# Kernel optimization log

Measured on AMD Instinct MI355X. Metric: run time of the kernel, lower is better.

The kernel has to match this reference:

```python
import jax, jax.numpy as jnp
import numpy as np

STATE_DIM = 1024
INPUT_DIM = 1024
OUTPUT_DIM = 1024
BATCH = 8
SEQ = 2048


def setup_inputs() -> dict:
    key = jax.random.key(0)
    k_x, k_a, k_b, k_w, k_bias = jax.random.split(key, 5)
    x = jax.random.normal(k_x, (BATCH, SEQ, INPUT_DIM), dtype=jnp.float32)
    # diagonal transition a in (0, 0.99) for stability
    A = jax.random.uniform(k_a, (STATE_DIM,), dtype=jnp.float32, minval=0.0, maxval=0.99)
    B = jax.random.normal(k_b, (STATE_DIM, INPUT_DIM), dtype=jnp.float32) / np.sqrt(INPUT_DIM)
    W = jax.random.normal(k_w, (OUTPUT_DIM, STATE_DIM), dtype=jnp.float32) / np.sqrt(STATE_DIM)
    b = jax.random.normal(k_bias, (OUTPUT_DIM,), dtype=jnp.float32) * 0.01
    return {"x": x, "A": A, "B": B, "W": W, "b": b}


def reference(x, A, B, W, b):
    # x: [batch, seq, input_dim]
    # Input projection: u_t = B x_t  -> [batch, seq, state_dim]
    u = jnp.einsum('bld,nd->bln', x, B)
    # Diagonal linear recurrence h_t = A * h_{t-1} + u_t via associative scan.
    # Pair representation (a, b) composes as (a1*a2, a2*b1 + b2).
    aa = jnp.broadcast_to(A, u.shape)

    def combine(c1, c2):
        a1, b1 = c1
        a2, b2 = c2
        return a1 * a2, a2 * b1 + b2

    _, h = jax.lax.associative_scan(combine, (aa, u), axis=1)
    # Output projection: [batch, seq, output_dim]
    return jnp.einsum('bln,on->blo', h, W) + b
```

## Files before the change

### kernel.cpp

```cpp
#include <hip/hip_runtime.h>
#include <stdint.h>

#define BATCH 8
#define SEQ 2048
#define DIM 1024
#define MTOT (BATCH * SEQ)
#define NCHUNK 32
#define CLEN (SEQ / NCHUNK)

typedef __attribute__((ext_vector_type(8))) short short8;
typedef __attribute__((ext_vector_type(4))) float floatx4;


__device__ __forceinline__ unsigned short f2bf(float f) {
  union { float f; unsigned u; } c; c.f = f;
  unsigned u = c.u;
  return (unsigned short)((u + 0x7FFFu + ((u >> 16) & 1u)) >> 16);
}
__device__ __forceinline__ float bf2f(unsigned short h) {
  union { unsigned u; float f; } c; c.u = ((unsigned)h) << 16;
  return c.f;
}

__device__ __forceinline__ void gll16(const void* g, void* l) {
  __builtin_amdgcn_global_load_lds(
      (__attribute__((address_space(1))) void*)(uintptr_t)g,
      (__attribute__((address_space(3))) void*)(uintptr_t)l,
      16, 0, 0);
}


__global__ __launch_bounds__(256) void cast_f32_bf16_kernel(
    const float* __restrict__ src, unsigned short* __restrict__ dst, int n8) {
  int i = blockIdx.x * 256 + threadIdx.x;
  if (i >= n8) return;
  const float4* s4 = (const float4*)src;
  float4 a = s4[2 * i], b = s4[2 * i + 1];
  uint4 o;
  o.x = (unsigned)f2bf(a.x) | ((unsigned)f2bf(a.y) << 16);
  o.y = (unsigned)f2bf(a.z) | ((unsigned)f2bf(a.w) << 16);
  o.z = (unsigned)f2bf(b.x) | ((unsigned)f2bf(b.y) << 16);
  o.w = (unsigned)f2bf(b.z) | ((unsigned)f2bf(b.w) << 16);
  ((uint4*)dst)[i] = o;
}


template <bool OUT_BF16>
__global__ __launch_bounds__(256) void gemm_nt(
    const unsigned short* __restrict__ A,
    const unsigned short* __restrict__ B,
    void* __restrict__ Cp,
    const float* __restrict__ bias,
    int K, int N) {
  __shared__ unsigned short sA[128 * 64];
  __shared__ unsigned short sB[128 * 64];

  const int tid = threadIdx.x;
  const int wave = tid >> 6, lane = tid & 63;
  const size_t m0 = (size_t)blockIdx.y * 128;
  const int n0 = blockIdx.x * 128;

  floatx4 acc[4][4] = {};

  const int srow = wave * 8 + (lane >> 3);
  const int scol = (lane & 7) * 8;
  const unsigned short* gA = A + (m0 + srow) * (size_t)K + scol;
  const unsigned short* gB = B + ((size_t)n0 + srow) * (size_t)K + scol;
  unsigned short* lA = sA + wave * 8 * 64;
  unsigned short* lB = sB + wave * 8 * 64;

  const int fr = lane & 15;
  const int fk = (lane >> 4) * 8;
  const int wm = (wave & 1) * 64, wn = (wave >> 1) * 64;

  for (int kt = 0; kt < K; kt += 64) {
#pragma unroll
    for (int r = 0; r < 4; ++r) {
      gll16(gA + (size_t)r * 32 * K + kt, lA + r * 32 * 64);
      gll16(gB + (size_t)r * 32 * K + kt, lB + r * 32 * 64);
    }
    asm volatile("s_waitcnt vmcnt(0)" ::: "memory");
    __syncthreads();
#pragma unroll
    for (int kk = 0; kk < 64; kk += 32) {
      short8 af[4], bfv[4];
#pragma unroll
      for (int i = 0; i < 4; ++i)
        af[i] = *(const short8*)(sA + (wm + i * 16 + fr) * 64 + kk + fk);
#pragma unroll
      for (int j = 0; j < 4; ++j)
        bfv[j] = *(const short8*)(sB + (wn + j * 16 + fr) * 64 + kk + fk);
#pragma unroll
      for (int i = 0; i < 4; ++i)
#pragma unroll
        for (int j = 0; j < 4; ++j)
          acc[i][j] = __builtin_amdgcn_mfma_f32_16x16x32_bf16(
              af[i], bfv[j], acc[i][j], 0, 0, 0);
    }
    __syncthreads();
  }

  const int col = lane & 15;
  const int row4 = (lane >> 4) * 4;
#pragma unroll
  for (int i = 0; i < 4; ++i) {
#pragma unroll
    for (int j = 0; j < 4; ++j) {
#pragma unroll
      for (int r = 0; r < 4; ++r) {
        size_t m = m0 + wm + i * 16 + row4 + r;
        int n = n0 + wn + j * 16 + col;
        float v = acc[i][j][r];
        if (OUT_BF16) {
          ((unsigned short*)Cp)[m * N + n] = f2bf(v);
        } else {
          ((float*)Cp)[m * N + n] = v + bias[n];
        }
      }
    }
  }
}


__global__ __launch_bounds__(256) void scan_carry(
    const unsigned short* __restrict__ u, const float* __restrict__ A,
    float* __restrict__ carry) {
  const int n = blockIdx.x * 256 + threadIdx.x;
  const int c = blockIdx.y;
  const int b = blockIdx.z;
  const float a = A[n];
  size_t base = ((size_t)(b * SEQ + c * CLEN)) * DIM + n;
  float s = 0.f;
#pragma unroll 8
  for (int t = 0; t < CLEN; ++t)
    s = fmaf(a, s, bf2f(u[base + (size_t)t * DIM]));
  carry[((size_t)b * NCHUNK + c) * DIM + n] = s;
}

__global__ __launch_bounds__(256) void scan_combine(
    float* __restrict__ carry, const float* __restrict__ A) {
  const int id = blockIdx.x * 256 + threadIdx.x;
  const int b = id >> 10, n = id & (DIM - 1);
  float a = A[n];
  float aL = a;
#pragma unroll
  for (int i = 0; i < 6; ++i) aL *= aL;
  float s = 0.f;
  for (int c = 0; c < NCHUNK; ++c) {
    size_t idx = ((size_t)b * NCHUNK + c) * DIM + n;
    float local = carry[idx];
    carry[idx] = s;
    s = fmaf(aL, s, local);
  }
}

__global__ __launch_bounds__(256) void scan_apply(
    unsigned short* __restrict__ u, const float* __restrict__ A,
    const float* __restrict__ carry) {
  const int n = blockIdx.x * 256 + threadIdx.x;
  const int c = blockIdx.y;
  const int b = blockIdx.z;
  const float a = A[n];
  float s = carry[((size_t)b * NCHUNK + c) * DIM + n];
  size_t base = ((size_t)(b * SEQ + c * CLEN)) * DIM + n;
#pragma unroll 8
  for (int t = 0; t < CLEN; ++t) {
    size_t idx = base + (size_t)t * DIM;
    s = fmaf(a, s, bf2f(u[idx]));
    u[idx] = f2bf(s);
  }
}


extern "C" void kernel_launch(void* const* d_in, const int* in_sizes, int n_in,
                              void* d_out, int out_size, void* d_ws,
                              size_t ws_size, hipStream_t stream) {
  const float* x    = (const float*)d_in[0];
  const float* A    = (const float*)d_in[1];
  const float* B    = (const float*)d_in[2];
  const float* W    = (const float*)d_in[3];
  const float* bias = (const float*)d_in[4];

  char* ws = (char*)d_ws;
  unsigned short* xb = (unsigned short*)ws;
  unsigned short* u  = (unsigned short*)(ws + 33554432);
  unsigned short* Bb = (unsigned short*)(ws + 67108864);
  unsigned short* Wb = (unsigned short*)(ws + 69206016);
  float* carry       = (float*)(ws + 71303168);

  cast_f32_bf16_kernel<<<(MTOT * DIM / 8) / 256, 256, 0, stream>>>(
      x, xb, MTOT * DIM / 8);
  cast_f32_bf16_kernel<<<(DIM * DIM / 8) / 256, 256, 0, stream>>>(
      B, Bb, DIM * DIM / 8);
  cast_f32_bf16_kernel<<<(DIM * DIM / 8) / 256, 256, 0, stream>>>(
      W, Wb, DIM * DIM / 8);

  gemm_nt<true><<<dim3(DIM / 128, MTOT / 128), 256, 0, stream>>>(
      xb, Bb, (void*)u, nullptr, DIM, DIM);

  scan_carry<<<dim3(DIM / 256, NCHUNK, BATCH), 256, 0, stream>>>(u, A, carry);
  scan_combine<<<dim3((BATCH * DIM) / 256), 256, 0, stream>>>(carry, A);
  scan_apply<<<dim3(DIM / 256, NCHUNK, BATCH), 256, 0, stream>>>(u, A, carry);

  gemm_nt<false><<<dim3(DIM / 128, MTOT / 128), 256, 0, stream>>>(
      u, Wb, d_out, bias, DIM, DIM);
}
```

Before: 257.7 us.

## Fuse casts, swizzle GEMM LDS, remap tiles per XCD, vectorize scan kernels

Merges the three cast kernels into one launch. The GEMM gets an XOR-swizzled LDS layout to cut bank conflicts, a 1D grid remapped so each XCD owns contiguous M tiles for L2 reuse, and a bf16 epilogue staged through LDS for coalesced 16-byte stores. The scan kernels now process 8 channels per thread with vector loads and stores, and the chunk count doubles to expose more parallelism. The carry buffer reuses the xb workspace region, which is safe only because xb is dead after the first GEMM.

```diff
diff --git a/kernel.cpp b/kernel.cpp
--- a/kernel.cpp
+++ b/kernel.cpp
@@ -5,10 +5,11 @@
 #define SEQ 2048
 #define DIM 1024
 #define MTOT (BATCH * SEQ)
-#define NCHUNK 32
+#define NCHUNK 64
 #define CLEN (SEQ / NCHUNK)
 
 typedef __attribute__((ext_vector_type(8))) short short8;
+typedef __attribute__((ext_vector_type(8))) unsigned short ushort8;
 typedef __attribute__((ext_vector_type(4))) float floatx4;
 
 
@@ -30,18 +31,32 @@
 }
 
 
-__global__ __launch_bounds__(256) void cast_f32_bf16_kernel(
-    const float* __restrict__ src, unsigned short* __restrict__ dst, int n8) {
+#define XN8 (MTOT * DIM / 8)
+#define MN8 (DIM * DIM / 8)
+
+__global__ __launch_bounds__(256) void cast3_kernel(
+    const float* __restrict__ x, const float* __restrict__ B,
+    const float* __restrict__ W, unsigned short* __restrict__ xb,
+    unsigned short* __restrict__ Bb, unsigned short* __restrict__ Wb) {
   int i = blockIdx.x * 256 + threadIdx.x;
-  if (i >= n8) return;
+  const float* src;
+  unsigned short* dst;
+  int li;
+  if (i < XN8) {
+    src = x; dst = xb; li = i;
+  } else if (i < XN8 + MN8) {
+    src = B; dst = Bb; li = i - XN8;
+  } else {
+    src = W; dst = Wb; li = i - XN8 - MN8;
+  }
   const float4* s4 = (const float4*)src;
-  float4 a = s4[2 * i], b = s4[2 * i + 1];
+  float4 a = s4[2 * li], b = s4[2 * li + 1];
   uint4 o;
   o.x = (unsigned)f2bf(a.x) | ((unsigned)f2bf(a.y) << 16);
   o.y = (unsigned)f2bf(a.z) | ((unsigned)f2bf(a.w) << 16);
   o.z = (unsigned)f2bf(b.x) | ((unsigned)f2bf(b.y) << 16);
   o.w = (unsigned)f2bf(b.z) | ((unsigned)f2bf(b.w) << 16);
-  ((uint4*)dst)[i] = o;
+  ((uint4*)dst)[li] = o;
 }
 
 
@@ -52,25 +67,32 @@
     void* __restrict__ Cp,
     const float* __restrict__ bias,
     int K, int N) {
-  __shared__ unsigned short sA[128 * 64];
-  __shared__ unsigned short sB[128 * 64];
+  __shared__ unsigned short smem[16384];
+  unsigned short* sA = smem;
+  unsigned short* sB = smem + 8192;
 
   const int tid = threadIdx.x;
   const int wave = tid >> 6, lane = tid & 63;
-  const size_t m0 = (size_t)blockIdx.y * 128;
-  const int n0 = blockIdx.x * 128;
+
+  const int id = blockIdx.x;
+  const int xcd = id & 7, j = id >> 3;
+  const int mt = xcd * 16 + (j >> 3);
+  const int nt = j & 7;
+  const size_t m0 = (size_t)mt * 128;
+  const int n0 = nt * 128;
 
   floatx4 acc[4][4] = {};
 
   const int srow = wave * 8 + (lane >> 3);
-  const int scol = (lane & 7) * 8;
+  const int scol = (((lane & 7) ^ ((lane >> 3) & 7)) * 8);
   const unsigned short* gA = A + (m0 + srow) * (size_t)K + scol;
   const unsigned short* gB = B + ((size_t)n0 + srow) * (size_t)K + scol;
   unsigned short* lA = sA + wave * 8 * 64;
   unsigned short* lB = sB + wave * 8 * 64;
 
   const int fr = lane & 15;
-  const int fk = (lane >> 4) * 8;
+  const int frs = fr & 7;
+  const int kb = lane >> 4;
   const int wm = (wave & 1) * 64, wn = (wave >> 1) * 64;
 
   for (int kt = 0; kt < K; kt += 64) {
@@ -86,35 +108,55 @@
       short8 af[4], bfv[4];
 #pragma unroll
       for (int i = 0; i < 4; ++i)
-        af[i] = *(const short8*)(sA + (wm + i * 16 + fr) * 64 + kk + fk);
-#pragma unroll
-      for (int j = 0; j < 4; ++j)
-        bfv[j] = *(const short8*)(sB + (wn + j * 16 + fr) * 64 + kk + fk);
+        af[i] = *(const short8*)(sA + (wm + i * 16 + fr) * 64 +
+                                 ((((kk >> 3) + kb) ^ frs) * 8));
+#pragma unroll
+      for (int jj = 0; jj < 4; ++jj)
+        bfv[jj] = *(const short8*)(sB + (wn + jj * 16 + fr) * 64 +
+                                   ((((kk >> 3) + kb) ^ frs) * 8));
 #pragma unroll
       for (int i = 0; i < 4; ++i)
 #pragma unroll
-        for (int j = 0; j < 4; ++j)
-          acc[i][j] = __builtin_amdgcn_mfma_f32_16x16x32_bf16(
-              af[i], bfv[j], acc[i][j], 0, 0, 0);
+        for (int jj = 0; jj < 4; ++jj)
+          acc[i][jj] = __builtin_amdgcn_mfma_f32_16x16x32_bf16(
+              af[i], bfv[jj], acc[i][jj], 0, 0, 0);
     }
     __syncthreads();
   }
 
   const int col = lane & 15;
   const int row4 = (lane >> 4) * 4;
-#pragma unroll
-  for (int i = 0; i < 4; ++i) {
-#pragma unroll
-    for (int j = 0; j < 4; ++j) {
-#pragma unroll
-      for (int r = 0; r < 4; ++r) {
-        size_t m = m0 + wm + i * 16 + row4 + r;
-        int n = n0 + wn + j * 16 + col;
-        float v = acc[i][j][r];
-        if (OUT_BF16) {
-          ((unsigned short*)Cp)[m * N + n] = f2bf(v);
-        } else {
-          ((float*)Cp)[m * N + n] = v + bias[n];
+
+  if (OUT_BF16) {
+    unsigned short* sC = smem;
+#pragma unroll
+    for (int i = 0; i < 4; ++i)
+#pragma unroll
+      for (int jj = 0; jj < 4; ++jj)
+#pragma unroll
+        for (int r = 0; r < 4; ++r)
+          sC[(wm + i * 16 + row4 + r) * 128 + wn + jj * 16 + col] =
+              f2bf(acc[i][jj][r]);
+    __syncthreads();
+    unsigned short* C = (unsigned short*)Cp;
+#pragma unroll
+    for (int s = 0; s < 8; ++s) {
+      int row = wave * 32 + s * 4 + (lane >> 4);
+      int c8 = (lane & 15) * 8;
+      *(ushort8*)(C + (m0 + row) * (size_t)N + n0 + c8) =
+          *(const ushort8*)(sC + row * 128 + c8);
+    }
+  } else {
+    float* C = (float*)Cp;
+#pragma unroll
+    for (int i = 0; i < 4; ++i) {
+#pragma unroll
+      for (int jj = 0; jj < 4; ++jj) {
+#pragma unroll
+        for (int r = 0; r < 4; ++r) {
+          size_t m = m0 + wm + i * 16 + row4 + r;
+          int n = n0 + wn + jj * 16 + col;
+          C[m * N + n] = acc[i][jj][r] + bias[n];
         }
       }
     }
@@ -125,16 +167,24 @@
 __global__ __launch_bounds__(256) void scan_carry(
     const unsigned short* __restrict__ u, const float* __restrict__ A,
     float* __restrict__ carry) {
-  const int n = blockIdx.x * 256 + threadIdx.x;
-  const int c = blockIdx.y;
-  const int b = blockIdx.z;
-  const float a = A[n];
-  size_t base = ((size_t)(b * SEQ + c * CLEN)) * DIM + n;
-  float s = 0.f;
-#pragma unroll 8
-  for (int t = 0; t < CLEN; ++t)
-    s = fmaf(a, s, bf2f(u[base + (size_t)t * DIM]));
-  carry[((size_t)b * NCHUNK + c) * DIM + n] = s;
+  const int n0 = threadIdx.x * 8;
+  const int c = blockIdx.x * 2 + threadIdx.y;
+  const int b = blockIdx.y;
+  float a[8], s[8];
+  *(float4*)&a[0] = *(const float4*)(A + n0);
+  *(float4*)&a[4] = *(const float4*)(A + n0 + 4);
+#pragma unroll
+  for (int i = 0; i < 8; ++i) s[i] = 0.f;
+  size_t base = ((size_t)(b * SEQ + c * CLEN)) * DIM + n0;
+#pragma unroll 4
+  for (int t = 0; t < CLEN; ++t) {
+    ushort8 v = *(const ushort8*)(u + base + (size_t)t * DIM);
+#pragma unroll
+    for (int i = 0; i < 8; ++i) s[i] = fmaf(a[i], s[i], bf2f(v[i]));
+  }
+  float* dst = carry + ((size_t)b * NCHUNK + c) * DIM + n0;
+  *(float4*)dst = *(float4*)&s[0];
+  *(float4*)(dst + 4) = *(float4*)&s[4];
 }
 
 __global__ __launch_bounds__(256) void scan_combine(
@@ -144,7 +194,7 @@
   float a = A[n];
   float aL = a;
 #pragma unroll
-  for (int i = 0; i < 6; ++i) aL *= aL;
+  for (int i = 0; i < 5; ++i) aL *= aL;
   float s = 0.f;
   for (int c = 0; c < NCHUNK; ++c) {
     size_t idx = ((size_t)b * NCHUNK + c) * DIM + n;
@@ -157,17 +207,27 @@
 __global__ __launch_bounds__(256) void scan_apply(
     unsigned short* __restrict__ u, const float* __restrict__ A,
     const float* __restrict__ carry) {
-  const int n = blockIdx.x * 256 + threadIdx.x;
-  const int c = blockIdx.y;
-  const int b = blockIdx.z;
-  const float a = A[n];
-  float s = carry[((size_t)b * NCHUNK + c) * DIM + n];
-  size_t base = ((size_t)(b * SEQ + c * CLEN)) * DIM + n;
-#pragma unroll 8
+  const int n0 = threadIdx.x * 8;
+  const int c = blockIdx.x * 2 + threadIdx.y;
+  const int b = blockIdx.y;
+  float a[8], s[8];
+  *(float4*)&a[0] = *(const float4*)(A + n0);
+  *(float4*)&a[4] = *(const float4*)(A + n0 + 4);
+  const float* cin = carry + ((size_t)b * NCHUNK + c) * DIM + n0;
+  *(float4*)&s[0] = *(const float4*)cin;
+  *(float4*)&s[4] = *(const float4*)(cin + 4);
+  size_t base = ((size_t)(b * SEQ + c * CLEN)) * DIM + n0;
+#pragma unroll 4
   for (int t = 0; t < CLEN; ++t) {
     size_t idx = base + (size_t)t * DIM;
-    s = fmaf(a, s, bf2f(u[idx]));
-    u[idx] = f2bf(s);
+    ushort8 v = *(const ushort8*)(u + idx);
+    ushort8 o;
+#pragma unroll
+    for (int i = 0; i < 8; ++i) {
+      s[i] = fmaf(a[i], s[i], bf2f(v[i]));
+      o[i] = f2bf(s[i]);
+    }
+    *(ushort8*)(u + idx) = o;
   }
 }
 
@@ -183,25 +243,20 @@
 
   char* ws = (char*)d_ws;
   unsigned short* xb = (unsigned short*)ws;
+  float* carry       = (float*)ws;
   unsigned short* u  = (unsigned short*)(ws + 33554432);
   unsigned short* Bb = (unsigned short*)(ws + 67108864);
   unsigned short* Wb = (unsigned short*)(ws + 69206016);
-  float* carry       = (float*)(ws + 71303168);
-
-  cast_f32_bf16_kernel<<<(MTOT * DIM / 8) / 256, 256, 0, stream>>>(
-      x, xb, MTOT * DIM / 8);
-  cast_f32_bf16_kernel<<<(DIM * DIM / 8) / 256, 256, 0, stream>>>(
-      B, Bb, DIM * DIM / 8);
-  cast_f32_bf16_kernel<<<(DIM * DIM / 8) / 256, 256, 0, stream>>>(
-      W, Wb, DIM * DIM / 8);
-
-  gemm_nt<true><<<dim3(DIM / 128, MTOT / 128), 256, 0, stream>>>(
+
+  cast3_kernel<<<(XN8 + 2 * MN8) / 256, 256, 0, stream>>>(x, B, W, xb, Bb, Wb);
+
+  gemm_nt<true><<<(MTOT / 128) * (DIM / 128), 256, 0, stream>>>(
       xb, Bb, (void*)u, nullptr, DIM, DIM);
 
-  scan_carry<<<dim3(DIM / 256, NCHUNK, BATCH), 256, 0, stream>>>(u, A, carry);
-  scan_combine<<<dim3((BATCH * DIM) / 256), 256, 0, stream>>>(carry, A);
-  scan_apply<<<dim3(DIM / 256, NCHUNK, BATCH), 256, 0, stream>>>(u, A, carry);
-
-  gemm_nt<false><<<dim3(DIM / 128, MTOT / 128), 256, 0, stream>>>(
+  scan_carry<<<dim3(NCHUNK / 2, BATCH), dim3(128, 2), 0, stream>>>(u, A, carry);
+  scan_combine<<<(BATCH * DIM) / 256, 256, 0, stream>>>(carry, A);
+  scan_apply<<<dim3(NCHUNK / 2, BATCH), dim3(128, 2), 0, stream>>>(u, A, carry);
+
+  gemm_nt<false><<<(MTOT / 128) * (DIM / 128), 256, 0, stream>>>(
       u, Wb, d_out, bias, DIM, DIM);
 }
```

After: 236.9 us. 1.09x faster.
